# Kernel optimization log

Measured on AMD Instinct MI355X. Metric: run time of the kernel, lower is better.

Reference implementation:

```python
import jax, jax.numpy as jnp
import numpy as np

B, T = 512, 8192
DT = jnp.float32(1e-3)


def setup_inputs() -> dict:
    key = jax.random.key(0)
    k1, k2, k3, k4 = jax.random.split(key, 4)
    # scale noise so the 8192-step linear recurrence stays well-conditioned
    xicovs = jax.random.normal(k1, (B, T, 2, 2), jnp.float32) * 0.05
    dy = jax.random.normal(k2, (B, T, 2), jnp.float32) * 0.05
    coeffs_A = jax.random.uniform(k3, (2, 2), jnp.float32, -0.05, 0.05)  # 'uniform' init kernel
    C = jax.random.normal(k4, (2, 2), jnp.float32)
    return {"xicovs": xicovs, "dy": dy, "coeffs_A": coeffs_A, "C": C}


def reference(xicovs, dy, coeffs_A, C):
    # xicovs: [B,T,2,2], dy: [B,T,2]
    Bv = xicovs.shape[0]
    # initial state [1,0] broadcast over batch
    x0 = jnp.broadcast_to(jnp.array([1.0, 0.0], jnp.float32), (Bv, 2))
    xi_t = jnp.swapaxes(xicovs, 0, 1)  # [T,B,2,2]
    dy_t = jnp.swapaxes(dy, 0, 1)      # [T,B,2]

    def step(x, inp):
        xic, dyt = inp  # [B,2,2], [B,2]
        # cell emits C @ x_prev * dt
        out = jnp.einsum('ij,bj->bi', C, x) * DT
        A_minus_xiC = coeffs_A - jnp.einsum('bij,jk->bik', xic, C)  # [B,2,2]
        dx = jnp.einsum('bij,bj->bi', A_minus_xiC, x) * DT + jnp.einsum('bij,bj->bi', xic, dyt)
        return x + dx, out

    _, outs = jax.lax.scan(step, x0, (xi_t, dy_t))  # outs: [T,B,2]
    return jnp.swapaxes(outs, 0, 1)  # [B,T,2] (return_sequences=True)
```

## Files before the change

kernel.cpp:

```cpp
#include <hip/hip_runtime.h>


#define B_   512
#define T_   8192
#define LPT  8
#define NT   1024
static_assert(NT * LPT == T_, "one block covers one batch");

#define SLICE_F4 128

struct Aff { float m00, m01, m10, m11, v0, v1; };

__device__ __forceinline__ Aff aff_compose(const Aff& L, const Aff& E) {
    Aff r;
    r.m00 = L.m00*E.m00 + L.m01*E.m10;
    r.m01 = L.m00*E.m01 + L.m01*E.m11;
    r.m10 = L.m10*E.m00 + L.m11*E.m10;
    r.m11 = L.m10*E.m01 + L.m11*E.m11;
    r.v0  = L.m00*E.v0  + L.m01*E.v1 + L.v0;
    r.v1  = L.m10*E.v0  + L.m11*E.v1 + L.v1;
    return r;
}

__device__ __forceinline__ Aff aff_identity() {
    Aff r; r.m00 = 1.f; r.m01 = 0.f; r.m10 = 0.f; r.m11 = 1.f; r.v0 = 0.f; r.v1 = 0.f;
    return r;
}

__global__ __launch_bounds__(NT, 4) void grm_fused(
    const float* __restrict__ xic, const float* __restrict__ dy,
    const float* __restrict__ Aptr, const float* __restrict__ Cptr,
    float4* __restrict__ out4)
{
    __shared__ float4 lds4[16 * SLICE_F4];

    const int b    = blockIdx.x;
    const int tid  = threadIdx.x;
    const int lane = tid & 63;
    const int wave = tid >> 6;

    float4* slice = lds4 + wave * SLICE_F4;

    const float DT = 1e-3f;
    const float cd00 = Cptr[0]*DT, cd01 = Cptr[1]*DT;
    const float cd10 = Cptr[2]*DT, cd11 = Cptr[3]*DT;
    const float i00 = 1.0f + Aptr[0]*DT, i01 = Aptr[1]*DT;
    const float i10 = Aptr[2]*DT,        i11 = 1.0f + Aptr[3]*DT;

    const int wbase = b * T_ + wave * 512;
    const float4* xw = (const float4*)xic + wbase;
    const float4* dw = (const float4*)dy  + (wbase >> 1);
    float4*       ow = out4 + (wbase >> 1);

    float4 t[8], u[4];
    #pragma unroll
    for (int j = 0; j < 8; ++j) t[j] = xw[j*64 + lane];
    #pragma unroll
    for (int j = 0; j < 4; ++j) u[j] = dw[j*64 + lane];

    float4 a[LPT];
    #pragma unroll
    for (int r = 0; r < 4; ++r) {
        #pragma unroll
        for (int jj = 0; jj < 2; ++jj) {
            int j = 2*r + jj;
            int f = j*64 + lane;
            int rel = (f >> 3) & 15;
            slice[rel*8 + ((lane & 7) ^ (rel & 7))] = t[j];
        }
        if ((lane >> 4) == r) {
            int rel = lane & 15;
            #pragma unroll
            for (int s = 0; s < LPT; ++s)
                a[s] = slice[rel*8 + (s ^ (rel & 7))];
        }
    }

    float4 d[4];
    #pragma unroll
    for (int r = 0; r < 2; ++r) {
        #pragma unroll
        for (int jj = 0; jj < 2; ++jj) {
            int j = 2*r + jj;
            int f = j*64 + lane;
            int rel = (f >> 2) & 31;
            slice[rel*4 + ((lane & 3) ^ (rel & 3))] = u[j];
        }
        if ((lane >> 5) == r) {
            int rel = lane & 31;
            #pragma unroll
            for (int s = 0; s < 4; ++s)
                d[s] = slice[rel*4 + (s ^ (rel & 3))];
        }
    }

#define STEP_MAP(i, S)                                                  \
    {                                                                   \
        const float4 x4 = a[i];                                         \
        const float dyx = ((i)&1) ? d[(i)>>1].z : d[(i)>>1].x;          \
        const float dyy = ((i)&1) ? d[(i)>>1].w : d[(i)>>1].y;          \
        (S).m00 = i00 - (x4.x*cd00 + x4.y*cd10);                        \
        (S).m01 = i01 - (x4.x*cd01 + x4.y*cd11);                        \
        (S).m10 = i10 - (x4.z*cd00 + x4.w*cd10);                        \
        (S).m11 = i11 - (x4.z*cd01 + x4.w*cd11);                        \
        (S).v0  = x4.x*dyx + x4.y*dyy;                                  \
        (S).v1  = x4.z*dyx + x4.w*dyy;                                  \
    }

    Aff P;
    STEP_MAP(0, P);
    #pragma unroll
    for (int i = 1; i < LPT; ++i) { Aff s; STEP_MAP(i, s); P = aff_compose(s, P); }

    Aff S = P;
    #pragma unroll
    for (int sh = 1; sh < 64; sh <<= 1) {
        Aff q;
        q.m00 = __shfl_up(S.m00, sh); q.m01 = __shfl_up(S.m01, sh);
        q.m10 = __shfl_up(S.m10, sh); q.m11 = __shfl_up(S.m11, sh);
        q.v0  = __shfl_up(S.v0,  sh); q.v1  = __shfl_up(S.v1,  sh);
        if (lane >= sh) S = aff_compose(S, q);
    }

    if (lane == 63) {
        float* h = (float*)slice;
        h[0] = S.m00; h[1] = S.m01; h[2] = S.m10; h[3] = S.m11;
        h[4] = S.v0;  h[5] = S.v1;
    }
    __syncthreads();

    Aff Ew = aff_identity();
    for (int w = 0; w < wave; ++w) {
        const float* h = (const float*)(lds4 + w * SLICE_F4);
        Aff t2;
        t2.m00 = h[0]; t2.m01 = h[1]; t2.m10 = h[2]; t2.m11 = h[3];
        t2.v0  = h[4]; t2.v1  = h[5];
        Ew = aff_compose(t2, Ew);
    }
    __syncthreads();

    Aff El;
    El.m00 = __shfl_up(S.m00, 1); El.m01 = __shfl_up(S.m01, 1);
    El.m10 = __shfl_up(S.m10, 1); El.m11 = __shfl_up(S.m11, 1);
    El.v0  = __shfl_up(S.v0,  1); El.v1  = __shfl_up(S.v1,  1);
    if (lane == 0) El = aff_identity();

    Aff E = aff_compose(El, Ew);
    float x0 = E.m00 + E.v0;
    float x1 = E.m10 + E.v1;

    float4 o4[4];
    #pragma unroll
    for (int i = 0; i < LPT; ++i) {
        float oxx = cd00*x0 + cd01*x1;
        float oyy = cd10*x0 + cd11*x1;
        if (i & 1) { o4[i>>1].z = oxx; o4[i>>1].w = oyy; }
        else       { o4[i>>1].x = oxx; o4[i>>1].y = oyy; }
        Aff s; STEP_MAP(i, s);
        float nx0 = s.m00*x0 + s.m01*x1 + s.v0;
        float nx1 = s.m10*x0 + s.m11*x1 + s.v1;
        x0 = nx0; x1 = nx1;
    }
#undef STEP_MAP

    #pragma unroll
    for (int r = 0; r < 2; ++r) {
        if ((lane >> 5) == r) {
            int rel = lane & 31;
            #pragma unroll
            for (int s = 0; s < 4; ++s)
                slice[rel*4 + (s ^ (rel & 3))] = o4[s];
        }
        #pragma unroll
        for (int jj = 0; jj < 2; ++jj) {
            int j = 2*r + jj;
            int f = j*64 + lane;
            int rel = (f >> 2) & 31;
            ow[f] = slice[rel*4 + ((lane & 3) ^ (rel & 3))];
        }
    }
}

extern "C" void kernel_launch(void* const* d_in, const int* in_sizes, int n_in,
                              void* d_out, int out_size, void* d_ws, size_t ws_size,
                              hipStream_t stream) {
    const float* xic  = (const float*)d_in[0];
    const float* dy   = (const float*)d_in[1];
    const float* Aptr = (const float*)d_in[2];
    const float* Cptr = (const float*)d_in[3];
    float4* out = (float4*)d_out;

    grm_fused<<<B_, NT, 0, stream>>>(xic, dy, Aptr, Cptr, out);
}
```

Before: 144.7 us.

## Process two batches per block and prefetch the second batch's inputs

Each 1024-thread block now handles two batch rows in sequence, launching half as many blocks. The second row's xicovs data is loaded up front, and its dy data is fetched into registers during the first row's scan, after the block barrier. The aim is to overlap global-memory latency for the second row with compute on the first. The cost is many more live registers per thread and fewer resident blocks, which may lower occupancy or cause spills.

```diff
diff --git a/kernel.cpp b/kernel.cpp
--- a/kernel.cpp
+++ b/kernel.cpp
@@ -5,6 +5,7 @@
 #define T_   8192
 #define LPT  8
 #define NT   1024
+#define NB   2
 static_assert(NT * LPT == T_, "one block covers one batch");
 
 #define SLICE_F4 128
@@ -26,73 +27,6 @@
     Aff r; r.m00 = 1.f; r.m01 = 0.f; r.m10 = 0.f; r.m11 = 1.f; r.v0 = 0.f; r.v1 = 0.f;
     return r;
 }
-
-__global__ __launch_bounds__(NT, 4) void grm_fused(
-    const float* __restrict__ xic, const float* __restrict__ dy,
-    const float* __restrict__ Aptr, const float* __restrict__ Cptr,
-    float4* __restrict__ out4)
-{
-    __shared__ float4 lds4[16 * SLICE_F4];
-
-    const int b    = blockIdx.x;
-    const int tid  = threadIdx.x;
-    const int lane = tid & 63;
-    const int wave = tid >> 6;
-
-    float4* slice = lds4 + wave * SLICE_F4;
-
-    const float DT = 1e-3f;
-    const float cd00 = Cptr[0]*DT, cd01 = Cptr[1]*DT;
-    const float cd10 = Cptr[2]*DT, cd11 = Cptr[3]*DT;
-    const float i00 = 1.0f + Aptr[0]*DT, i01 = Aptr[1]*DT;
-    const float i10 = Aptr[2]*DT,        i11 = 1.0f + Aptr[3]*DT;
-
-    const int wbase = b * T_ + wave * 512;
-    const float4* xw = (const float4*)xic + wbase;
-    const float4* dw = (const float4*)dy  + (wbase >> 1);
-    float4*       ow = out4 + (wbase >> 1);
-
-    float4 t[8], u[4];
-    #pragma unroll
-    for (int j = 0; j < 8; ++j) t[j] = xw[j*64 + lane];
-    #pragma unroll
-    for (int j = 0; j < 4; ++j) u[j] = dw[j*64 + lane];
-
-    float4 a[LPT];
-    #pragma unroll
-    for (int r = 0; r < 4; ++r) {
-        #pragma unroll
-        for (int jj = 0; jj < 2; ++jj) {
-            int j = 2*r + jj;
-            int f = j*64 + lane;
-            int rel = (f >> 3) & 15;
-            slice[rel*8 + ((lane & 7) ^ (rel & 7))] = t[j];
-        }
-        if ((lane >> 4) == r) {
-            int rel = lane & 15;
-            #pragma unroll
-            for (int s = 0; s < LPT; ++s)
-                a[s] = slice[rel*8 + (s ^ (rel & 7))];
-        }
-    }
-
-    float4 d[4];
-    #pragma unroll
-    for (int r = 0; r < 2; ++r) {
-        #pragma unroll
-        for (int jj = 0; jj < 2; ++jj) {
-            int j = 2*r + jj;
-            int f = j*64 + lane;
-            int rel = (f >> 2) & 31;
-            slice[rel*4 + ((lane & 3) ^ (rel & 3))] = u[j];
-        }
-        if ((lane >> 5) == r) {
-            int rel = lane & 31;
-            #pragma unroll
-            for (int s = 0; s < 4; ++s)
-                d[s] = slice[rel*4 + (s ^ (rel & 3))];
-        }
-    }
 
 #define STEP_MAP(i, S)                                                  \
     {                                                                   \
@@ -107,6 +41,52 @@
         (S).v1  = x4.z*dyx + x4.w*dyy;                                  \
     }
 
+template<bool PREFETCH_DY>
+__device__ __forceinline__ void process_batch(
+    float4 (&t)[8], float4 (&u)[4],
+    float4* __restrict__ slice, float4* __restrict__ lds4,
+    const int lane, const int wave,
+    const float cd00, const float cd01, const float cd10, const float cd11,
+    const float i00, const float i01, const float i10, const float i11,
+    float4* __restrict__ ow,
+    const float4* __restrict__ dw_next, float4 (&u_next)[4])
+{
+    float4 a[LPT];
+    #pragma unroll
+    for (int r = 0; r < 4; ++r) {
+        #pragma unroll
+        for (int jj = 0; jj < 2; ++jj) {
+            int j = 2*r + jj;
+            int f = j*64 + lane;
+            int rel = (f >> 3) & 15;
+            slice[rel*8 + ((lane & 7) ^ (rel & 7))] = t[j];
+        }
+        if ((lane >> 4) == r) {
+            int rel = lane & 15;
+            #pragma unroll
+            for (int s = 0; s < LPT; ++s)
+                a[s] = slice[rel*8 + (s ^ (rel & 7))];
+        }
+    }
+
+    float4 d[4];
+    #pragma unroll
+    for (int r = 0; r < 2; ++r) {
+        #pragma unroll
+        for (int jj = 0; jj < 2; ++jj) {
+            int j = 2*r + jj;
+            int f = j*64 + lane;
+            int rel = (f >> 2) & 31;
+            slice[rel*4 + ((lane & 3) ^ (rel & 3))] = u[j];
+        }
+        if ((lane >> 5) == r) {
+            int rel = lane & 31;
+            #pragma unroll
+            for (int s = 0; s < 4; ++s)
+                d[s] = slice[rel*4 + (s ^ (rel & 3))];
+        }
+    }
+
     Aff P;
     STEP_MAP(0, P);
     #pragma unroll
@@ -138,6 +118,11 @@
         Ew = aff_compose(t2, Ew);
     }
     __syncthreads();
+
+    if constexpr (PREFETCH_DY) {
+        #pragma unroll
+        for (int j = 0; j < 4; ++j) u_next[j] = dw_next[j*64 + lane];
+    }
 
     Aff El;
     El.m00 = __shfl_up(S.m00, 1); El.m01 = __shfl_up(S.m01, 1);
@@ -161,7 +146,6 @@
         float nx1 = s.m10*x0 + s.m11*x1 + s.v1;
         x0 = nx0; x1 = nx1;
     }
-#undef STEP_MAP
 
     #pragma unroll
     for (int r = 0; r < 2; ++r) {
@@ -180,6 +164,54 @@
         }
     }
 }
+
+__global__ __launch_bounds__(NT, 4) void grm_fused(
+    const float* __restrict__ xic, const float* __restrict__ dy,
+    const float* __restrict__ Aptr, const float* __restrict__ Cptr,
+    float4* __restrict__ out4)
+{
+    __shared__ float4 lds4[16 * SLICE_F4];
+
+    const int tid  = threadIdx.x;
+    const int lane = tid & 63;
+    const int wave = tid >> 6;
+
+    float4* slice = lds4 + wave * SLICE_F4;
+
+    const float DT = 1e-3f;
+    const float cd00 = Cptr[0]*DT, cd01 = Cptr[1]*DT;
+    const float cd10 = Cptr[2]*DT, cd11 = Cptr[3]*DT;
+    const float i00 = 1.0f + Aptr[0]*DT, i01 = Aptr[1]*DT;
+    const float i10 = Aptr[2]*DT,        i11 = 1.0f + Aptr[3]*DT;
+
+    const int b0     = blockIdx.x * NB;
+    const int wbase0 = b0 * T_ + wave * 512;
+    const int wbase1 = wbase0 + T_;
+    const float4* xw0 = (const float4*)xic + wbase0;
+    const float4* dw0 = (const float4*)dy  + (wbase0 >> 1);
+    float4*       ow0 = out4 + (wbase0 >> 1);
+    const float4* xw1 = (const float4*)xic + wbase1;
+    const float4* dw1 = (const float4*)dy  + (wbase1 >> 1);
+    float4*       ow1 = out4 + (wbase1 >> 1);
+
+    float4 t0[8], u0[4], t1[8], u1[4];
+    #pragma unroll
+    for (int j = 0; j < 8; ++j) t0[j] = xw0[j*64 + lane];
+    #pragma unroll
+    for (int j = 0; j < 4; ++j) u0[j] = dw0[j*64 + lane];
+    #pragma unroll
+    for (int j = 0; j < 8; ++j) t1[j] = xw1[j*64 + lane];
+
+    process_batch<true>(t0, u0, slice, lds4, lane, wave,
+                        cd00, cd01, cd10, cd11, i00, i01, i10, i11,
+                        ow0, dw1, u1);
+
+    process_batch<false>(t1, u1, slice, lds4, lane, wave,
+                         cd00, cd01, cd10, cd11, i00, i01, i10, i11,
+                         ow1, dw1, u1);
+}
+
+#undef STEP_MAP
 
 extern "C" void kernel_launch(void* const* d_in, const int* in_sizes, int n_in,
                               void* d_out, int out_size, void* d_ws, size_t ws_size,
@@ -190,5 +222,5 @@
     const float* Cptr = (const float*)d_in[3];
     float4* out = (float4*)d_out;
 
-    grm_fused<<<B_, NT, 0, stream>>>(xic, dy, Aptr, Cptr, out);
-}
+    grm_fused<<<B_ / NB, NT, 0, stream>>>(xic, dy, Aptr, Cptr, out);
+}
```

Result: slower. 168.5 us (+16.5%).
